# Performance work log

Hardware: AMD Instinct MI355X
Metric: run time of the kernel (lower is better)

Reference implementation:

```python
import jax, jax.numpy as jnp
import numpy as np

B, C, H, W = 4, 256, 64, 64
CQK = C // 8  # query/key projection dim = 32


def setup_inputs() -> dict:
    key = jax.random.key(0)
    ks = jax.random.split(key, 9)
    inp = {
        "input": jax.random.normal(ks[0], (B, C, H, W), dtype=jnp.float32),
        "structure": jax.random.normal(ks[1], (B, C, H, W), dtype=jnp.float32),
        "style": jax.random.normal(ks[2], (B, C, H, W), dtype=jnp.float32),
        # 1x1 conv weights stored as [out, in] (kernel spatial dims are 1)
        "Wq": jax.random.normal(ks[3], (CQK, C), dtype=jnp.float32) * (1.0 / np.sqrt(C)),
        "bq": jax.random.normal(ks[4], (CQK,), dtype=jnp.float32) * 0.01,
        "Wk": jax.random.normal(ks[5], (CQK, C), dtype=jnp.float32) * (1.0 / np.sqrt(C)),
        "bk": jax.random.normal(ks[6], (CQK,), dtype=jnp.float32) * 0.01,
        "Wv": jax.random.normal(ks[7], (C, C), dtype=jnp.float32) * (1.0 / np.sqrt(C)),
        "bv": jax.random.normal(ks[8], (C,), dtype=jnp.float32) * 0.01,
    }
    return inp


def reference(input, structure, style, Wq, bq, Wk, bk, Wv, bv):
    b, c, h, w = input.shape
    n = h * w
    # 1x1 convs == per-pixel channel GEMMs
    q = jnp.einsum('bchw,oc->bohw', input, Wq) + bq[None, :, None, None]
    k = jnp.einsum('bchw,oc->bohw', structure, Wk) + bk[None, :, None, None]
    v = jnp.einsum('bchw,oc->bohw', style, Wv) + bv[None, :, None, None]
    q = q.reshape(b, -1, n).transpose(0, 2, 1)   # [B, N, CQK]
    k = k.reshape(b, -1, n)                      # [B, CQK, N]
    v = v.reshape(b, -1, n)                      # [B, C, N]
    scores = jnp.einsum('bnc,bcm->bnm', q, k)    # [B, N, N], no 1/sqrt(d) scaling (as in source)
    # source subtracts the GLOBAL max of the score tensor (scalar), then softmax(dim=-1)
    attn = jax.nn.softmax(scores - jnp.max(scores), axis=-1)
    # out = value @ attn^T : out[b,c,i] = sum_j v[b,c,j] * attn[b,i,j]
    out = jnp.einsum('bcj,bij->bci', v, attn)
    return out.reshape(b, c, h, w)
```

## Files before the change

### kernel.cpp

```cpp
#include <hip/hip_runtime.h>
#include <hip/hip_bf16.h>
#include <math.h>

typedef __attribute__((ext_vector_type(8))) short short8;
typedef __attribute__((ext_vector_type(4))) short short4v;
typedef __attribute__((ext_vector_type(4))) float f32x4;

#define LOG2E 1.44269504088896f

__device__ __forceinline__ unsigned short f2bf(float f) {
  union { float f; unsigned int u; } v; v.f = f;
  unsigned int r = v.u + 0x7fffu + ((v.u >> 16) & 1u);
  return (unsigned short)(r >> 16);
}
__device__ __forceinline__ float bf2f(unsigned short h) {
  union { unsigned int u; float f; } v; v.u = ((unsigned int)h) << 16;
  return v.f;
}

__global__ void k_wtrans(const float* __restrict__ Wq, const float* __restrict__ Wk,
                         float* __restrict__ wt) {
  for (int i = threadIdx.x; i < 32 * 256; i += 256) {
    int d = i >> 8, c = i & 255;
    wt[c * 64 + d] = Wq[i];
    wt[c * 64 + 32 + d] = Wk[i];
  }
}

__global__ __launch_bounds__(256) void k_qkproj(
    const float* __restrict__ input, const float* __restrict__ structure,
    const float* __restrict__ wt, const float* __restrict__ bq, const float* __restrict__ bk,
    unsigned short* __restrict__ qh, unsigned short* __restrict__ ql,
    unsigned short* __restrict__ kh) {
  __shared__ float red[2 * 64 * 65];
  const int b = blockIdx.y;
  const int n0 = blockIdx.x * 64;
  const int wu = __builtin_amdgcn_readfirstlane(threadIdx.x >> 6);
  const int l = threadIdx.x & 63;
  const size_t ibase = ((size_t)b << 20) + (size_t)(n0 + l);

  float aq[32], ak[32];
#pragma unroll
  for (int d = 0; d < 32; ++d) { aq[d] = 0.f; ak[d] = 0.f; }

#pragma unroll 2
  for (int cc = 0; cc < 64; ++cc) {
    const int c = wu * 64 + cc;
    const float xq = input[ibase + ((size_t)c << 12)];
    const float xk = structure[ibase + ((size_t)c << 12)];
    const float* wr = wt + c * 64;
#pragma unroll
    for (int d = 0; d < 32; ++d) {
      aq[d] = fmaf(wr[d], xq, aq[d]);
      ak[d] = fmaf(wr[32 + d], xk, ak[d]);
    }
  }
  float* myred = red + ((wu & 1) * 64 + l) * 65;
  if (wu < 2) {
#pragma unroll
    for (int d = 0; d < 32; ++d) { myred[d] = aq[d]; myred[32 + d] = ak[d]; }
  }
  __syncthreads();
  if (wu >= 2) {
#pragma unroll
    for (int d = 0; d < 32; ++d) { myred[d] += aq[d]; myred[32 + d] += ak[d]; }
  }
  __syncthreads();

  const int p = threadIdx.x & 63;
  const int half = (threadIdx.x >> 6) & 1;
  const int dh = threadIdx.x >> 7;
  const float* bias = half ? bk : bq;
  const float scl = half ? 1.0f : LOG2E;
  unsigned short hs[16], lo[16];
#pragma unroll
  for (int d2 = 0; d2 < 16; ++d2) {
    const int d = dh * 16 + d2;
    float v = red[p * 65 + half * 32 + d] + red[(64 + p) * 65 + half * 32 + d];
    v = (v + bias[d]) * scl;
    unsigned short h = f2bf(v);
    hs[d2] = h;
    lo[d2] = f2bf(v - bf2f(h));
  }
  const size_t row = ((size_t)b << 12) + (size_t)(n0 + p);
  if (!half) {
    unsigned short* dsth = qh + row * 32 + dh * 16;
    unsigned short* dstl = ql + row * 32 + dh * 16;
#pragma unroll
    for (int i2 = 0; i2 < 2; ++i2) {
      uint4 t, t2;
      t.x = (unsigned)hs[i2*8+0] | ((unsigned)hs[i2*8+1] << 16);
      t.y = (unsigned)hs[i2*8+2] | ((unsigned)hs[i2*8+3] << 16);
      t.z = (unsigned)hs[i2*8+4] | ((unsigned)hs[i2*8+5] << 16);
      t.w = (unsigned)hs[i2*8+6] | ((unsigned)hs[i2*8+7] << 16);
      t2.x = (unsigned)lo[i2*8+0] | ((unsigned)lo[i2*8+1] << 16);
      t2.y = (unsigned)lo[i2*8+2] | ((unsigned)lo[i2*8+3] << 16);
      t2.z = (unsigned)lo[i2*8+4] | ((unsigned)lo[i2*8+5] << 16);
      t2.w = (unsigned)lo[i2*8+6] | ((unsigned)lo[i2*8+7] << 16);
      ((uint4*)dsth)[i2] = t;
      ((uint4*)dstl)[i2] = t2;
    }
  } else {
    unsigned short* dsth = kh + row * 32 + dh * 16;
#pragma unroll
    for (int i2 = 0; i2 < 2; ++i2) {
      uint4 t;
      t.x = (unsigned)hs[i2*8+0] | ((unsigned)hs[i2*8+1] << 16);
      t.y = (unsigned)hs[i2*8+2] | ((unsigned)hs[i2*8+3] << 16);
      t.z = (unsigned)hs[i2*8+4] | ((unsigned)hs[i2*8+5] << 16);
      t.w = (unsigned)hs[i2*8+6] | ((unsigned)hs[i2*8+7] << 16);
      ((uint4*)dsth)[i2] = t;
    }
  }
}

__global__ __launch_bounds__(256) void k_caststyle(const float* __restrict__ style,
                                                   unsigned short* __restrict__ xs) {
  const int b = blockIdx.z, ct = blockIdx.y;
  const int n = blockIdx.x * 256 + threadIdx.x;
  const float* src = style + ((size_t)b << 20) + (((size_t)(ct * 64)) << 12) + (size_t)n;
  unsigned short* dst = xs + (((size_t)b << 12) + (size_t)n) * 256 + ct * 64;
#pragma unroll
  for (int gq = 0; gq < 8; ++gq) {
    uint4 t;
    unsigned vv[4];
#pragma unroll
    for (int q2 = 0; q2 < 4; ++q2) {
      unsigned short a = f2bf(src[((size_t)(gq * 8 + q2 * 2)) << 12]);
      unsigned short bb = f2bf(src[((size_t)(gq * 8 + q2 * 2 + 1)) << 12]);
      vv[q2] = (unsigned)a | ((unsigned)bb << 16);
    }
    t.x = vv[0]; t.y = vv[1]; t.z = vv[2]; t.w = vv[3];
    *(uint4*)(dst + gq * 8) = t;
  }
}

__global__ __launch_bounds__(256) void k_vgemm(const unsigned short* __restrict__ xs,
                                               const float* __restrict__ Wv,
                                               const float* __restrict__ bv,
                                               unsigned short* __restrict__ vws) {
  const int b = blockIdx.z, coT = blockIdx.y, nT = blockIdx.x;
  const int w = threadIdx.x >> 6, l = threadIdx.x & 63;
  const int m = l & 15, g = l >> 4;
  const int co0 = coT * 64 + w * 16;
  const int n0 = nT * 128;
  f32x4 acc[8];
#pragma unroll
  for (int f = 0; f < 8; ++f) { acc[f][0]=0.f; acc[f][1]=0.f; acc[f][2]=0.f; acc[f][3]=0.f; }

#pragma unroll 2
  for (int kc = 0; kc < 8; ++kc) {
    const int c0 = kc * 32 + g * 8;
    const float* wp = Wv + (size_t)(co0 + m) * 256 + c0;
    float4 a0 = *(const float4*)wp;
    float4 a1 = *(const float4*)(wp + 4);
    short8 af;
    af[0]=(short)f2bf(a0.x); af[1]=(short)f2bf(a0.y); af[2]=(short)f2bf(a0.z); af[3]=(short)f2bf(a0.w);
    af[4]=(short)f2bf(a1.x); af[5]=(short)f2bf(a1.y); af[6]=(short)f2bf(a1.z); af[7]=(short)f2bf(a1.w);
#pragma unroll
    for (int f = 0; f < 8; ++f) {
      const short8 bfr = *(const short8*)(xs + (((size_t)b << 12) + (size_t)(n0 + f * 16 + m)) * 256 + c0);
      acc[f] = __builtin_amdgcn_mfma_f32_16x16x32_bf16(af, bfr, acc[f], 0, 0, 0);
    }
  }
  float4 bvv = *(const float4*)(bv + co0 + g * 4);
  const float bvr[4] = {bvv.x, bvv.y, bvv.z, bvv.w};
#pragma unroll
  for (int f = 0; f < 8; ++f)
#pragma unroll
    for (int r = 0; r < 4; ++r) {
      const int co = co0 + g * 4 + r;
      const int n = n0 + f * 16 + m;
      vws[(((size_t)(b * 256 + co)) << 12) + n] = f2bf(acc[f][r] + bvr[r]);
    }
}

#define P_PANEL  16384
#define P_BUF    32768
#define LDS_TOT  65536

__global__ __launch_bounds__(256) void k_flash(
    const unsigned short* __restrict__ qh_ws, const unsigned short* __restrict__ ql_ws,
    const unsigned short* __restrict__ kh_ws, const unsigned short* __restrict__ v_ws,
    float* __restrict__ out0, unsigned short* __restrict__ pacc1,
    float* __restrict__ pl) {
  __shared__ char lds[LDS_TOT];
  const int bid = blockIdx.x;
  const int qt = bid >> 3;
  const int b = (bid >> 1) & 3;
  const int jh = bid & 1;
  const int tid = threadIdx.x;
  const int wu = __builtin_amdgcn_readfirstlane(tid >> 6);
  const int l = tid & 63;
  const int m = l & 15, g = l >> 4;

  const size_t qrowA = (((size_t)b << 12) + (size_t)(qt * 128 + wu * 32 + m)) * 32 + g * 8;
  const size_t qrowB = (((size_t)b << 12) + (size_t)(qt * 128 + wu * 32 + 16 + m)) * 32 + g * 8;
  const short8 qhfA = *(const short8*)(qh_ws + qrowA);
  const short8 qlfA = *(const short8*)(ql_ws + qrowA);
  const short8 qhfB = *(const short8*)(qh_ws + qrowB);
  const short8 qlfB = *(const short8*)(ql_ws + qrowB);

  f32x4 acc[8][4];
#pragma unroll
  for (int it = 0; it < 8; ++it)
#pragma unroll
    for (int ct = 0; ct < 4; ++ct) { acc[it][ct][0]=0.f; acc[it][ct][1]=0.f; acc[it][ct][2]=0.f; acc[it][ct][3]=0.f; }
  float lsum[2][4];
#pragma unroll
  for (int grp = 0; grp < 2; ++grp)
#pragma unroll
    for (int r = 0; r < 4; ++r) lsum[grp][r] = 0.f;

  const int jbase = jh * 2048;
  for (int jt = 0; jt < 16; ++jt) {
    const int j128 = jbase + jt * 128;
    const int pb = jt & 1;
    char* Pb = lds + pb * P_BUF;
    short8 vbf[4][4];
#pragma unroll
    for (int ks = 0; ks < 4; ++ks)
#pragma unroll
      for (int ct = 0; ct < 4; ++ct)
        vbf[ks][ct] = *(const short8*)(v_ws +
          (((size_t)(b * 256 + wu * 64 + ct * 16 + m)) << 12) + j128 + ks * 32 + g * 8);
    short8 khv[8];
#pragma unroll
    for (int t = 0; t < 8; ++t)
      khv[t] = *(const short8*)(kh_ws + (((size_t)b << 12) + (size_t)(j128 + t * 16 + m)) * 32 + g * 8);
#pragma unroll
    for (int grp = 0; grp < 2; ++grp) {
      const short8 qh_f = grp ? qhfB : qhfA;
      const short8 ql_f = grp ? qlfB : qlfA;
      f32x4 sv[8];
#pragma unroll
      for (int t = 0; t < 8; ++t) {
        f32x4 z = {0.f, 0.f, 0.f, 0.f};
        f32x4 s0 = __builtin_amdgcn_mfma_f32_16x16x32_bf16(qh_f, khv[t], z, 0, 0, 0);
        sv[t] = __builtin_amdgcn_mfma_f32_16x16x32_bf16(ql_f, khv[t], s0, 0, 0, 0);
      }
#pragma unroll
      for (int t = 0; t < 8; ++t)
#pragma unroll
        for (int r = 0; r < 4; ++r) {
          const float p = exp2f(sv[t][r]);
          lsum[grp][r] += p;
          const int row = wu * 32 + grp * 16 + g * 4 + r;
          const int cw2 = (t & 3) * 32 + 2 * m;
          *(unsigned short*)(Pb + (t >> 2) * P_PANEL + row * 128 + (cw2 ^ ((row & 7) << 4))) = f2bf(p);
        }
    }
    __syncthreads();
#pragma unroll
    for (int ks = 0; ks < 4; ++ks) {
      short8 pa[8];
#pragma unroll
      for (int it = 0; it < 8; ++it) {
        const int row = it * 16 + m;
        pa[it] = *(const short8*)(Pb + (ks >> 1) * P_PANEL + row * 128 +
                                  (((ks & 1) * 64 + g * 16) ^ ((row & 7) << 4)));
      }
#pragma unroll
      for (int ct = 0; ct < 4; ++ct)
#pragma unroll
        for (int it = 0; it < 8; ++it)
          acc[it][ct] = __builtin_amdgcn_mfma_f32_16x16x32_bf16(pa[it], vbf[ks][ct], acc[it][ct], 0, 0, 0);
    }
  }
#pragma unroll
  for (int d = 1; d <= 8; d <<= 1)
#pragma unroll
    for (int grp = 0; grp < 2; ++grp)
#pragma unroll
      for (int r = 0; r < 4; ++r) lsum[grp][r] += __shfl_xor(lsum[grp][r], d);
  if (m == 0) {
#pragma unroll
    for (int grp = 0; grp < 2; ++grp)
#pragma unroll
      for (int r = 0; r < 4; ++r) {
        const int row = qt * 128 + wu * 32 + grp * 16 + g * 4 + r;
        pl[(size_t)jh * 16384 + ((size_t)b << 12) + row] = lsum[grp][r];
      }
  }
  if (jh == 0) {
#pragma unroll
    for (int it = 0; it < 8; ++it)
#pragma unroll
      for (int ct = 0; ct < 4; ++ct) {
        const int c = wu * 64 + ct * 16 + m;
        float4 o;
        o.x = acc[it][ct][0]; o.y = acc[it][ct][1]; o.z = acc[it][ct][2]; o.w = acc[it][ct][3];
        *(float4*)(out0 + (((size_t)(b * 256 + c)) << 12) + qt * 128 + it * 16 + g * 4) = o;
      }
  } else {
#pragma unroll
    for (int it = 0; it < 8; ++it)
#pragma unroll
      for (int ct = 0; ct < 4; ++ct) {
        const int c = wu * 64 + ct * 16 + m;
        short4v o;
        o[0] = (short)f2bf(acc[it][ct][0]); o[1] = (short)f2bf(acc[it][ct][1]);
        o[2] = (short)f2bf(acc[it][ct][2]); o[3] = (short)f2bf(acc[it][ct][3]);
        *(short4v*)(pacc1 + (((size_t)(b * 256 + c)) << 12) + qt * 128 + it * 16 + g * 4) = o;
      }
  }
}

__global__ __launch_bounds__(256) void k_combine(float* o, const unsigned short* __restrict__ pacc1,
                                                 const float* __restrict__ pl) {
  const int b = blockIdx.y;
  const int n = blockIdx.x * 64 + (threadIdx.x & 63);
  const int c0 = (threadIdx.x >> 6) * 64;
  const size_t mi = ((size_t)b << 12) + n;
  const float rl = 1.0f / (pl[mi] + pl[16384 + mi]);
#pragma unroll 4
  for (int ci = 0; ci < 64; ++ci) {
    const size_t a = (((size_t)(b * 256 + c0 + ci)) << 12) + n;
    o[a] = (o[a] + bf2f(pacc1[a])) * rl;
  }
}

extern "C" void kernel_launch(void* const* d_in, const int* in_sizes, int n_in,
                              void* d_out, int out_size, void* d_ws, size_t ws_size,
                              hipStream_t stream) {
  (void)in_sizes; (void)n_in; (void)out_size; (void)ws_size;
  const float* input     = (const float*)d_in[0];
  const float* structure = (const float*)d_in[1];
  const float* style     = (const float*)d_in[2];
  const float* Wq = (const float*)d_in[3];
  const float* bq = (const float*)d_in[4];
  const float* Wk = (const float*)d_in[5];
  const float* bk = (const float*)d_in[6];
  const float* Wv = (const float*)d_in[7];
  const float* bv = (const float*)d_in[8];
  float* out = (float*)d_out;
  char* ws = (char*)d_ws;

  float* wt           = (float*)(ws);
  unsigned short* qh  = (unsigned short*)(ws + 65536);
  unsigned short* ql  = (unsigned short*)(ws + 65536 + 1048576);
  unsigned short* kh  = (unsigned short*)(ws + 65536 + 2097152);
  unsigned short* vw  = (unsigned short*)(ws + 65536 + 3145728);
  unsigned short* xs  = (unsigned short*)(ws + 65536 + 3145728 + 8388608);
  unsigned short* pacc1 = xs;
  float* pl           = (float*)(ws + 20119552);

  k_wtrans<<<dim3(1), dim3(256), 0, stream>>>(Wq, Wk, wt);
  k_qkproj<<<dim3(64, 4), dim3(256), 0, stream>>>(input, structure, wt, bq, bk, qh, ql, kh);
  k_caststyle<<<dim3(16, 4, 4), dim3(256), 0, stream>>>(style, xs);
  k_vgemm<<<dim3(32, 4, 4), dim3(256), 0, stream>>>(xs, Wv, bv, vw);
  k_flash<<<dim3(256), dim3(256), 0, stream>>>(qh, ql, kh, vw, out, pacc1, pl);
  k_combine<<<dim3(64, 4), dim3(256), 0, stream>>>(out, pacc1, pl);
}
```

Baseline: 161.4 us.

## Split flash kernel work across 8 waves with fewer rows and channels each

The flash-attention kernel now launches 512 threads (8 wavefronts) per block instead of 4. Each wave computes scores for 16 query rows instead of 32 and accumulates 32 output channels instead of 64, which halves the per-wave accumulator and V-fragment register footprint. The aim is more waves per CU to hide latency of the MFMA, exp and global loads. In exchange, each block issues more redundant K loads per wave, and the grid has 256 blocks, which may limit how much extra occupancy is actually reached.

New measurement: 149.2 us. -7.5%, faster.

```diff
diff --git a/kernel.cpp b/kernel.cpp
--- a/kernel.cpp
+++ b/kernel.cpp
@@ -179,7 +179,7 @@
 #define P_BUF    32768
 #define LDS_TOT  65536
 
-__global__ __launch_bounds__(256) void k_flash(
+__global__ __launch_bounds__(512, 2) void k_flash(
     const unsigned short* __restrict__ qh_ws, const unsigned short* __restrict__ ql_ws,
     const unsigned short* __restrict__ kh_ws, const unsigned short* __restrict__ v_ws,
     float* __restrict__ out0, unsigned short* __restrict__ pacc1,
@@ -190,66 +190,56 @@
   const int b = (bid >> 1) & 3;
   const int jh = bid & 1;
   const int tid = threadIdx.x;
-  const int wu = __builtin_amdgcn_readfirstlane(tid >> 6);
+  const int w = __builtin_amdgcn_readfirstlane(tid >> 6);
   const int l = tid & 63;
   const int m = l & 15, g = l >> 4;
 
-  const size_t qrowA = (((size_t)b << 12) + (size_t)(qt * 128 + wu * 32 + m)) * 32 + g * 8;
-  const size_t qrowB = (((size_t)b << 12) + (size_t)(qt * 128 + wu * 32 + 16 + m)) * 32 + g * 8;
-  const short8 qhfA = *(const short8*)(qh_ws + qrowA);
-  const short8 qlfA = *(const short8*)(ql_ws + qrowA);
-  const short8 qhfB = *(const short8*)(qh_ws + qrowB);
-  const short8 qlfB = *(const short8*)(ql_ws + qrowB);
-
-  f32x4 acc[8][4];
+  const size_t qrow = (((size_t)b << 12) + (size_t)(qt * 128 + w * 16 + m)) * 32 + g * 8;
+  const short8 qhf = *(const short8*)(qh_ws + qrow);
+  const short8 qlf = *(const short8*)(ql_ws + qrow);
+
+  f32x4 acc[8][2];
 #pragma unroll
   for (int it = 0; it < 8; ++it)
 #pragma unroll
-    for (int ct = 0; ct < 4; ++ct) { acc[it][ct][0]=0.f; acc[it][ct][1]=0.f; acc[it][ct][2]=0.f; acc[it][ct][3]=0.f; }
-  float lsum[2][4];
-#pragma unroll
-  for (int grp = 0; grp < 2; ++grp)
-#pragma unroll
-    for (int r = 0; r < 4; ++r) lsum[grp][r] = 0.f;
+    for (int ct = 0; ct < 2; ++ct) { acc[it][ct][0]=0.f; acc[it][ct][1]=0.f; acc[it][ct][2]=0.f; acc[it][ct][3]=0.f; }
+  float lsum[4];
+#pragma unroll
+  for (int r = 0; r < 4; ++r) lsum[r] = 0.f;
 
   const int jbase = jh * 2048;
   for (int jt = 0; jt < 16; ++jt) {
     const int j128 = jbase + jt * 128;
     const int pb = jt & 1;
     char* Pb = lds + pb * P_BUF;
-    short8 vbf[4][4];
+    short8 vbf[4][2];
 #pragma unroll
     for (int ks = 0; ks < 4; ++ks)
 #pragma unroll
-      for (int ct = 0; ct < 4; ++ct)
+      for (int ct = 0; ct < 2; ++ct)
         vbf[ks][ct] = *(const short8*)(v_ws +
-          (((size_t)(b * 256 + wu * 64 + ct * 16 + m)) << 12) + j128 + ks * 32 + g * 8);
+          (((size_t)(b * 256 + w * 32 + ct * 16 + m)) << 12) + j128 + ks * 32 + g * 8);
     short8 khv[8];
 #pragma unroll
     for (int t = 0; t < 8; ++t)
       khv[t] = *(const short8*)(kh_ws + (((size_t)b << 12) + (size_t)(j128 + t * 16 + m)) * 32 + g * 8);
-#pragma unroll
-    for (int grp = 0; grp < 2; ++grp) {
-      const short8 qh_f = grp ? qhfB : qhfA;
-      const short8 ql_f = grp ? qlfB : qlfA;
-      f32x4 sv[8];
-#pragma unroll
-      for (int t = 0; t < 8; ++t) {
-        f32x4 z = {0.f, 0.f, 0.f, 0.f};
-        f32x4 s0 = __builtin_amdgcn_mfma_f32_16x16x32_bf16(qh_f, khv[t], z, 0, 0, 0);
-        sv[t] = __builtin_amdgcn_mfma_f32_16x16x32_bf16(ql_f, khv[t], s0, 0, 0, 0);
+    f32x4 sv[8];
+#pragma unroll
+    for (int t = 0; t < 8; ++t) {
+      f32x4 z = {0.f, 0.f, 0.f, 0.f};
+      f32x4 s0 = __builtin_amdgcn_mfma_f32_16x16x32_bf16(qhf, khv[t], z, 0, 0, 0);
+      sv[t] = __builtin_amdgcn_mfma_f32_16x16x32_bf16(qlf, khv[t], s0, 0, 0, 0);
+    }
+#pragma unroll
+    for (int t = 0; t < 8; ++t)
+#pragma unroll
+      for (int r = 0; r < 4; ++r) {
+        const float p = exp2f(sv[t][r]);
+        lsum[r] += p;
+        const int row = w * 16 + g * 4 + r;
+        const int cw2 = (t & 3) * 32 + 2 * m;
+        *(unsigned short*)(Pb + (t >> 2) * P_PANEL + row * 128 + (cw2 ^ ((row & 7) << 4))) = f2bf(p);
       }
-#pragma unroll
-      for (int t = 0; t < 8; ++t)
-#pragma unroll
-        for (int r = 0; r < 4; ++r) {
-          const float p = exp2f(sv[t][r]);
-          lsum[grp][r] += p;
-          const int row = wu * 32 + grp * 16 + g * 4 + r;
-          const int cw2 = (t & 3) * 32 + 2 * m;
-          *(unsigned short*)(Pb + (t >> 2) * P_PANEL + row * 128 + (cw2 ^ ((row & 7) << 4))) = f2bf(p);
-        }
-    }
     __syncthreads();
 #pragma unroll
     for (int ks = 0; ks < 4; ++ks) {
@@ -261,7 +251,7 @@
                                   (((ks & 1) * 64 + g * 16) ^ ((row & 7) << 4)));
       }
 #pragma unroll
-      for (int ct = 0; ct < 4; ++ct)
+      for (int ct = 0; ct < 2; ++ct)
 #pragma unroll
         for (int it = 0; it < 8; ++it)
           acc[it][ct] = __builtin_amdgcn_mfma_f32_16x16x32_bf16(pa[it], vbf[ks][ct], acc[it][ct], 0, 0, 0);
@@ -270,24 +260,20 @@
 #pragma unroll
   for (int d = 1; d <= 8; d <<= 1)
 #pragma unroll
-    for (int grp = 0; grp < 2; ++grp)
-#pragma unroll
-      for (int r = 0; r < 4; ++r) lsum[grp][r] += __shfl_xor(lsum[grp][r], d);
+    for (int r = 0; r < 4; ++r) lsum[r] += __shfl_xor(lsum[r], d);
   if (m == 0) {
 #pragma unroll
-    for (int grp = 0; grp < 2; ++grp)
-#pragma unroll
-      for (int r = 0; r < 4; ++r) {
-        const int row = qt * 128 + wu * 32 + grp * 16 + g * 4 + r;
-        pl[(size_t)jh * 16384 + ((size_t)b << 12) + row] = lsum[grp][r];
-      }
+    for (int r = 0; r < 4; ++r) {
+      const int row = qt * 128 + w * 16 + g * 4 + r;
+      pl[(size_t)jh * 16384 + ((size_t)b << 12) + row] = lsum[r];
+    }
   }
   if (jh == 0) {
 #pragma unroll
     for (int it = 0; it < 8; ++it)
 #pragma unroll
-      for (int ct = 0; ct < 4; ++ct) {
-        const int c = wu * 64 + ct * 16 + m;
+      for (int ct = 0; ct < 2; ++ct) {
+        const int c = w * 32 + ct * 16 + m;
         float4 o;
         o.x = acc[it][ct][0]; o.y = acc[it][ct][1]; o.z = acc[it][ct][2]; o.w = acc[it][ct][3];
         *(float4*)(out0 + (((size_t)(b * 256 + c)) << 12) + qt * 128 + it * 16 + g * 4) = o;
@@ -296,8 +282,8 @@
 #pragma unroll
     for (int it = 0; it < 8; ++it)
 #pragma unroll
-      for (int ct = 0; ct < 4; ++ct) {
-        const int c = wu * 64 + ct * 16 + m;
+      for (int ct = 0; ct < 2; ++ct) {
+        const int c = w * 32 + ct * 16 + m;
         short4v o;
         o[0] = (short)f2bf(acc[it][ct][0]); o[1] = (short)f2bf(acc[it][ct][1]);
         o[2] = (short)f2bf(acc[it][ct][2]); o[3] = (short)f2bf(acc[it][ct][3]);
@@ -349,6 +335,6 @@
   k_qkproj<<<dim3(64, 4), dim3(256), 0, stream>>>(input, structure, wt, bq, bk, qh, ql, kh);
   k_caststyle<<<dim3(16, 4, 4), dim3(256), 0, stream>>>(style, xs);
   k_vgemm<<<dim3(32, 4, 4), dim3(256), 0, stream>>>(xs, Wv, bv, vw);
-  k_flash<<<dim3(256), dim3(256), 0, stream>>>(qh, ql, kh, vw, out, pacc1, pl);
+  k_flash<<<dim3(256), dim3(512), 0, stream>>>(qh, ql, kh, vw, out, pacc1, pl);
   k_combine<<<dim3(64, 4), dim3(256), 0, stream>>>(out, pacc1, pl);
 }
```
